# Performance work log

Hardware: AMD Instinct MI355X
Metric: run time of the kernel (lower is better)

Reference implementation:

```python
import jax, jax.numpy as jnp
import numpy as np

B, C, H, W, K = 32, 256, 56, 56, 4


def setup_inputs() -> dict:
    key = jax.random.key(0)
    k0, k1, k2, k3, k4 = jax.random.split(key, 5)
    return {
        "x0": jax.random.normal(k0, (B, C, H, W), dtype=jnp.float32),
        "x1": jax.random.normal(k1, (B, C, H, W), dtype=jnp.float32),
        "x2": jax.random.normal(k2, (B, C, H, W), dtype=jnp.float32),
        "x3": jax.random.normal(k3, (B, C, H, W), dtype=jnp.float32),
        "attn_logits": jax.random.normal(k4, (K, B, C), dtype=jnp.float32),
    }


def reference(x0, x1, x2, x3, attn_logits):
    # Stack K branches: [K, B, C, H, W]
    xs = jnp.stack([x0, x1, x2, x3], axis=0)
    # Op (1): U = sum over branches, S = global average pool over H,W -> [B, C]
    u = xs.sum(axis=0)                      # [B, C, H, W]
    s = u.mean(axis=(2, 3))                 # [B, C]
    # Op (2): per-(b,c) softmax over the K branch logits, then weighted fuse
    w = jax.nn.softmax(attn_logits, axis=0)  # [K, B, C]
    out = jnp.einsum("kbc,kbchw->bchw", w, xs)  # [B, C, H, W]
    # u_sum (HW-sum of U) as written by the fused kernel when write_usum=true
    u_sum = u.sum(axis=(2, 3))              # [B, C]
    return out, s, u_sum
```

## Files before the change

kernel.cpp:

```cpp
#include <hip/hip_runtime.h>

constexpr int B = 32, C = 256, H = 56, W = 56, K = 4;
constexpr int HW = H * W;
constexpr int BC = B * C;
constexpr long long IMG = (long long)BC * HW;

__global__ __launch_bounds__(256) void sk_fuse_kernel(
    const float* __restrict__ x0, const float* __restrict__ x1,
    const float* __restrict__ x2, const float* __restrict__ x3,
    const float* __restrict__ logits,
    float* __restrict__ out,
    float* __restrict__ s_out,
    float* __restrict__ usum_out)
{
    const int bc = blockIdx.x;

    const float l0 = logits[0 * BC + bc];
    const float l1 = logits[1 * BC + bc];
    const float l2 = logits[2 * BC + bc];
    const float l3 = logits[3 * BC + bc];
    const float m  = fmaxf(fmaxf(l0, l1), fmaxf(l2, l3));
    const float e0 = expf(l0 - m);
    const float e1 = expf(l1 - m);
    const float e2 = expf(l2 - m);
    const float e3 = expf(l3 - m);
    const float inv = 1.0f / (e0 + e1 + e2 + e3);
    const float w0 = e0 * inv, w1 = e1 * inv, w2 = e2 * inv, w3 = e3 * inv;

    const size_t base = (size_t)bc * HW;
    const float4* __restrict__ p0 = (const float4*)(x0 + base);
    const float4* __restrict__ p1 = (const float4*)(x1 + base);
    const float4* __restrict__ p2 = (const float4*)(x2 + base);
    const float4* __restrict__ p3 = (const float4*)(x3 + base);
    float4* __restrict__ po = (float4*)(out + base);

    constexpr int NV = HW / 4;
    float usum = 0.0f;

    for (int i = threadIdx.x; i < NV; i += 256) {
        const float4 a = p0[i];
        const float4 b = p1[i];
        const float4 c = p2[i];
        const float4 d = p3[i];
        float4 o;
        o.x = w0 * a.x + w1 * b.x + w2 * c.x + w3 * d.x;
        o.y = w0 * a.y + w1 * b.y + w2 * c.y + w3 * d.y;
        o.z = w0 * a.z + w1 * b.z + w2 * c.z + w3 * d.z;
        o.w = w0 * a.w + w1 * b.w + w2 * c.w + w3 * d.w;
        po[i] = o;
        usum += (a.x + b.x + c.x + d.x)
              + (a.y + b.y + c.y + d.y)
              + (a.z + b.z + c.z + d.z)
              + (a.w + b.w + c.w + d.w);
    }

    #pragma unroll
    for (int off = 32; off > 0; off >>= 1)
        usum += __shfl_down(usum, off, 64);

    __shared__ float wsum[4];
    const int lane = threadIdx.x & 63;
    const int wid  = threadIdx.x >> 6;
    if (lane == 0) wsum[wid] = usum;
    __syncthreads();
    if (threadIdx.x == 0) {
        const float t = wsum[0] + wsum[1] + wsum[2] + wsum[3];
        usum_out[bc] = t;
        s_out[bc]    = t * (1.0f / HW);
    }
}

extern "C" void kernel_launch(void* const* d_in, const int* in_sizes, int n_in,
                              void* d_out, int out_size, void* d_ws, size_t ws_size,
                              hipStream_t stream) {
    const float* x0     = (const float*)d_in[0];
    const float* x1     = (const float*)d_in[1];
    const float* x2     = (const float*)d_in[2];
    const float* x3     = (const float*)d_in[3];
    const float* logits = (const float*)d_in[4];

    float* out      = (float*)d_out;
    float* s_out    = out + IMG;
    float* usum_out = s_out + BC;

    sk_fuse_kernel<<<BC, 256, 0, stream>>>(x0, x1, x2, x3, logits,
                                           out, s_out, usum_out);
}
```

Baseline: 102.4 us.

## Map one wavefront per channel with full unroll and nontemporal stores

Each wavefront now handles one (b,c) channel instead of a whole block, so the shared-memory reduction and block barrier are gone and only a wave shuffle reduction remains. The HW loop is fully unrolled into 12 full iterations plus a 16-lane tail, which exposes more independent loads per thread. Outputs are written with nontemporal stores to avoid polluting cache. The grid shrinks by four, and heavier per-thread register use could lower occupancy.

Result: no change. 103.0 us (+0.6%).

```diff
diff --git a/kernel.cpp b/kernel.cpp
--- a/kernel.cpp
+++ b/kernel.cpp
@@ -4,6 +4,8 @@
 constexpr int HW = H * W;
 constexpr int BC = B * C;
 constexpr long long IMG = (long long)BC * HW;
+
+typedef float f4 __attribute__((ext_vector_type(4)));
 
 __global__ __launch_bounds__(256) void sk_fuse_kernel(
     const float* __restrict__ x0, const float* __restrict__ x1,
@@ -13,7 +15,9 @@
     float* __restrict__ s_out,
     float* __restrict__ usum_out)
 {
-    const int bc = blockIdx.x;
+    const int lane = threadIdx.x & 63;
+    const int wid  = threadIdx.x >> 6;
+    const int bc   = (blockIdx.x << 2) + wid;
 
     const float l0 = logits[0 * BC + bc];
     const float l1 = logits[1 * BC + bc];
@@ -28,45 +32,50 @@
     const float w0 = e0 * inv, w1 = e1 * inv, w2 = e2 * inv, w3 = e3 * inv;
 
     const size_t base = (size_t)bc * HW;
-    const float4* __restrict__ p0 = (const float4*)(x0 + base);
-    const float4* __restrict__ p1 = (const float4*)(x1 + base);
-    const float4* __restrict__ p2 = (const float4*)(x2 + base);
-    const float4* __restrict__ p3 = (const float4*)(x3 + base);
-    float4* __restrict__ po = (float4*)(out + base);
+    const f4* __restrict__ p0 = (const f4*)(x0 + base);
+    const f4* __restrict__ p1 = (const f4*)(x1 + base);
+    const f4* __restrict__ p2 = (const f4*)(x2 + base);
+    const f4* __restrict__ p3 = (const f4*)(x3 + base);
+    f4* __restrict__ po = (f4*)(out + base);
 
-    constexpr int NV = HW / 4;
     float usum = 0.0f;
 
-    for (int i = threadIdx.x; i < NV; i += 256) {
-        const float4 a = p0[i];
-        const float4 b = p1[i];
-        const float4 c = p2[i];
-        const float4 d = p3[i];
-        float4 o;
+    auto fuse = [&](const f4& a, const f4& b,
+                    const f4& c, const f4& d) -> f4 {
+        f4 o;
         o.x = w0 * a.x + w1 * b.x + w2 * c.x + w3 * d.x;
         o.y = w0 * a.y + w1 * b.y + w2 * c.y + w3 * d.y;
         o.z = w0 * a.z + w1 * b.z + w2 * c.z + w3 * d.z;
         o.w = w0 * a.w + w1 * b.w + w2 * c.w + w3 * d.w;
-        po[i] = o;
         usum += (a.x + b.x + c.x + d.x)
               + (a.y + b.y + c.y + d.y)
               + (a.z + b.z + c.z + d.z)
               + (a.w + b.w + c.w + d.w);
+        return o;
+    };
+
+    #pragma unroll
+    for (int j = 0; j < 12; ++j) {
+        const int i = lane + (j << 6);
+        const f4 a = p0[i], b = p1[i], c = p2[i], d = p3[i];
+        const f4 o = fuse(a, b, c, d);
+        __builtin_nontemporal_store(o, &po[i]);
+    }
+
+    if (lane < 16) {
+        const int i = 768 + lane;
+        const f4 a = p0[i], b = p1[i], c = p2[i], d = p3[i];
+        const f4 o = fuse(a, b, c, d);
+        __builtin_nontemporal_store(o, &po[i]);
     }
 
     #pragma unroll
     for (int off = 32; off > 0; off >>= 1)
         usum += __shfl_down(usum, off, 64);
 
-    __shared__ float wsum[4];
-    const int lane = threadIdx.x & 63;
-    const int wid  = threadIdx.x >> 6;
-    if (lane == 0) wsum[wid] = usum;
-    __syncthreads();
-    if (threadIdx.x == 0) {
-        const float t = wsum[0] + wsum[1] + wsum[2] + wsum[3];
-        usum_out[bc] = t;
-        s_out[bc]    = t * (1.0f / HW);
+    if (lane == 0) {
+        __builtin_nontemporal_store(usum, &usum_out[bc]);
+        __builtin_nontemporal_store(usum * (1.0f / HW), &s_out[bc]);
     }
 }
 
@@ -83,6 +92,6 @@
     float* s_out    = out + IMG;
     float* usum_out = s_out + BC;
 
-    sk_fuse_kernel<<<BC, 256, 0, stream>>>(x0, x1, x2, x3, logits,
-                                           out, s_out, usum_out);
+    sk_fuse_kernel<<<BC / 4, 256, 0, stream>>>(x0, x1, x2, x3, logits,
+                                               out, s_out, usum_out);
 }
```
